# Kernel optimization log

Measured on AMD Instinct MI355X. Metric: run time of the kernel, lower is better.

## Reference

```python
import jax, jax.numpy as jnp
import numpy as np

E, H, V = 512, 1024, 32000
T_IN, T_DEC, B = 128, 128, 64
SOS = 1
WIPE_IDS = jnp.array([2, 3, 4])  # <EOS>, '\u56fe', '\u6298'


def gru_cell(x, h, Wih, Whh, bih, bhh):
    # torch nn.GRU cell math
    gi = x @ Wih.T + bih  # [B, 3H]
    gh = h @ Whh.T + bhh  # [B, 3H]
    i_r, i_z, i_n = jnp.split(gi, 3, axis=-1)
    h_r, h_z, h_n = jnp.split(gh, 3, axis=-1)
    r = jax.nn.sigmoid(i_r + h_r)
    z = jax.nn.sigmoid(i_z + h_z)
    n = jnp.tanh(i_n + r * h_n)
    return (1.0 - z) * n + z * h


def setup_inputs() -> dict:
    key = jax.random.key(0)
    ks = jax.random.split(key, 20)
    f = lambda k, shape: jax.random.normal(k, shape, jnp.float32) * 0.05
    inp = {
        'emb': f(ks[0], (V, E)),
        'enc_Wih': f(ks[1], (3 * H, E)), 'enc_Whh': f(ks[2], (3 * H, H)),
        'enc_bih': f(ks[3], (3 * H,)), 'enc_bhh': f(ks[4], (3 * H,)),
        'attn_W': f(ks[5], (T_IN, E + H)), 'attn_b': f(ks[6], (T_IN,)),
        'comb_W': f(ks[7], (H, E + H)), 'comb_b': f(ks[8], (H,)),
        'dec_Wih': f(ks[9], (3 * H, H)), 'dec_Whh': f(ks[10], (3 * H, H)),
        'dec_bih': f(ks[11], (3 * H,)), 'dec_bhh': f(ks[12], (3 * H,)),
        'out_W': f(ks[13], (V, H)), 'out_b': f(ks[14], (V,)),
        'src_tokens': jax.random.randint(ks[15], (B, T_IN), 0, V, jnp.int32),
        'tgt_tokens': jax.random.randint(ks[16], (B, T_DEC), 0, V, jnp.int32),
    }
    # pack_padded_sequence needs lengths sorted descending with max == T_IN
    sl = jax.random.randint(ks[17], (B,), 1, T_IN + 1, jnp.int32).at[0].set(T_IN)
    inp['src_lengths'] = jnp.sort(sl)[::-1]
    tl = jax.random.randint(ks[18], (B,), 1, T_DEC + 1, jnp.int32).at[0].set(T_DEC)
    inp['tgt_lengths'] = tl
    return inp


def reference(emb, enc_Wih, enc_Whh, enc_bih, enc_bhh, attn_W, attn_b,
              comb_W, comb_b, dec_Wih, dec_Whh, dec_bih, dec_bhh,
              out_W, out_b, src_tokens, src_lengths, tgt_tokens, tgt_lengths):
    # ---------------- Encoder (packed GRU semantics) ----------------
    x = emb[src_tokens]  # [B, T_IN, E]  (dropout is eval-mode identity)
    valid = jnp.arange(T_IN)[None, :] < src_lengths[:, None]  # [B, T_IN]

    def enc_step(h, inp):
        xt, vt = inp  # [B,E], [B]
        hn = gru_cell(xt, h, enc_Wih, enc_Whh, enc_bih, enc_bhh)
        h = jnp.where(vt[:, None], hn, h)          # freeze hidden past length
        out = jnp.where(vt[:, None], hn, 0.0)      # pad_packed zeros past length
        return h, out

    h0 = jnp.zeros((B, H), emb.dtype)
    enc_h, enc_out = jax.lax.scan(enc_step, h0, (x.transpose(1, 0, 2), valid.T))
    enc_out = enc_out.transpose(1, 0, 2)  # [B, T_IN, H]
    enc_out = jax.nn.log_softmax(enc_out, axis=1)  # LogSoftmax(dim=1) over time, as in source

    # ---------------- Attention decoder with teacher forcing ----------------
    sos = jnp.full((B,), SOS, src_tokens.dtype)

    def dec_step(carry, inp):
        h, prev = carry
        di, tgt_t = inp
        e = emb[prev]  # [B, E]
        union = jnp.concatenate([e, h], axis=-1)  # [B, E+H]
        aw = jax.nn.softmax(union @ attn_W.T + attn_b, axis=-1)  # [B, T_IN]
        info = jnp.einsum('bt,bth->bh', aw, enc_out)  # bmm
        comb = jax.nn.relu(jnp.concatenate([e, info], axis=-1) @ comb_W.T + comb_b)
        h = gru_cell(comb, h, dec_Wih, dec_Whh, dec_bih, dec_bhh)
        logits = h @ out_W.T + out_b  # [B, V]
        m = di < tgt_lengths  # [B] wipeEOS condition: now_len < length[i]
        wiped = jnp.where(m[:, None], 0.0, logits[:, WIPE_IDS])
        logits = logits.at[:, WIPE_IDS].set(wiped)
        pred_t = jnp.argmax(logits, axis=-1)
        ce = -jax.nn.log_softmax(logits, axis=-1)[jnp.arange(B), tgt_t]
        mf = m.astype(logits.dtype)
        step_loss = jnp.sum(ce * mf) / jnp.sum(mf)  # masked_select(...).mean()
        return (h, tgt_t), (pred_t, step_loss)

    (_, _), (preds, losses) = jax.lax.scan(
        dec_step, (enc_h, sos), (jnp.arange(T_DEC), tgt_tokens.T))
    return preds.T, jnp.sum(losses)
```

## Files before the change

kernel.cpp:

```cpp
#include <hip/hip_runtime.h>
#include <math.h>

typedef long long i64;

#define B_    64
#define TIN   128
#define TDEC  128
#define E_    512
#define H_    1024
#define V_    32000
#define H3    3072
#define EH    1536
#define NROWS 8192

__device__ inline unsigned int ordf(float v) {
  unsigned int u = __float_as_uint(v);
  return (u & 0x80000000u) ? ~u : (u | 0x80000000u);
}

__global__ void diag_fill(float* __restrict__ out, int n, float val) {
  int i = blockIdx.x * blockDim.x + threadIdx.x;
  if (i < n) out[i] = val;
}

__global__ void init_ws(float* __restrict__ hbuf, unsigned long long* __restrict__ amaxkey,
                        float* __restrict__ sumexp) {
  int i = blockIdx.x * blockDim.x + threadIdx.x;
  if (i < 2 * B_ * H_) hbuf[i] = 0.f;
  if (i < NROWS) { amaxkey[i] = 0ull; sumexp[i] = 0.f; }
}

__global__ void prep_tokens(const int* __restrict__ src, const int* __restrict__ tgt,
                            int* __restrict__ tok_src, int* __restrict__ tok_prev) {
  int r = blockIdx.x * blockDim.x + threadIdx.x;
  if (r >= NROWS) return;
  int t = r >> 6, b = r & 63;
  tok_src[r]  = src[b * TIN + t];
  tok_prev[r] = (t == 0) ? 1 : tgt[b * TDEC + (t - 1)];
}

__global__ __launch_bounds__(256)
void gemm_gather(const float* __restrict__ emb, const int* __restrict__ tok,
                 const float* __restrict__ W, int wstride,
                 const float* __restrict__ bias,
                 float* __restrict__ C, int ldc) {
  __shared__ float As[32][132];
  __shared__ float Bs[32][136];
  __shared__ int toks[128];
  const int tid = threadIdx.x;
  const int tx = tid & 15, ty = tid >> 4;
// ... 15 lines not shown
      As[k4 + 0][m] = v.x; As[k4 + 1][m] = v.y; As[k4 + 2][m] = v.z; As[k4 + 3][m] = v.w;
      float4 u = *reinterpret_cast<const float4*>(&W[(i64)(n0 + m) * wstride + k0 + k4]);
      Bs[k4 + 0][m] = u.x; Bs[k4 + 1][m] = u.y; Bs[k4 + 2][m] = u.z; Bs[k4 + 3][m] = u.w;
    }
    __syncthreads();
#pragma unroll
    for (int k = 0; k < 32; ++k) {
      float a[8], b[8];
      *(float4*)&a[0] = *(float4*)&As[k][ty * 4];
      *(float4*)&a[4] = *(float4*)&As[k][64 + ty * 4];
      *(float4*)&b[0] = *(float4*)&Bs[k][tx * 4];
      *(float4*)&b[4] = *(float4*)&Bs[k][64 + tx * 4];
#pragma unroll
      for (int i = 0; i < 8; ++i)
#pragma unroll
        for (int j = 0; j < 8; ++j)
          acc[i][j] = fmaf(a[i], b[j], acc[i][j]);
    }
    __syncthreads();
  }
#pragma unroll
  for (int i = 0; i < 8; ++i) {
    int rl = (i < 4) ? (ty * 4 + i) : (64 + ty * 4 + i - 4);
    int r = r0 + rl;
#pragma unroll
    for (int j = 0; j < 8; ++j) {
      int cl = (j < 4) ? (tx * 4 + j) : (64 + tx * 4 + j - 4);
      int c = n0 + cl;
      C[(i64)r * ldc + c] = acc[i][j] + bias[c];
    }
  }
}

template<int MODE>
__global__ __launch_bounds__(256)
void enc_step(const float* __restrict__ h_prev, float* __restrict__ h_next,
              const float* __restrict__ XGi,
              const float* __restrict__ emb, const int* __restrict__ src_tok,
              const float* __restrict__ Wih, const float* __restrict__ Whh,
              const float* __restrict__ bih, const float* __restrict__ bhh,
              const int* __restrict__ src_len,
              float* __restrict__ EncRaw, int t) {
  __shared__ float hs[64][66];
  __shared__ float Ws[3][8][66];
  __shared__ int toks[64];
  const int tid = threadIdx.x;
  const int n = tid & 7, q = tid >> 3;
  const int b0 = q * 2;
  const int n0 = blockIdx.x * 8;
  float gr0 = 0, gr1 = 0, gz0 = 0, gz1 = 0, gn0 = 0, gn1 = 0;
  float ir0 = 0, ir1 = 0, iz0 = 0, iz1 = 0, in0 = 0, in1 = 0;

  if (MODE == 1) {
    if (tid < 64) toks[tid] = src_tok[tid * TIN + t];
    __syncthreads();
    for (int k0 = 0; k0 < E_; k0 += 64) {
#pragma unroll
      for (int j = 0; j < 4; ++j) {
        int s = tid + 256 * j;
        int b = s >> 4, k4 = (s & 15) << 2;
        float4 v = *reinterpret_cast<const float4*>(&emb[(i64)toks[b] * E_ + k0 + k4]);
        hs[k4 + 0][b] = v.x; hs[k4 + 1][b] = v.y; hs[k4 + 2][b] = v.z; hs[k4 + 3][b] = v.w;
      }
#pragma unroll
      for (int j = 0; j < 2; ++j) {
        int s = tid + 256 * j;
        if (s < 384) {
          int g = s >> 7, s2 = s & 127;
          int nn = s2 >> 4, k4 = (s2 & 15) << 2;
          float4 v = *reinterpret_cast<const float4*>(&Wih[(i64)(g * H_ + n0 + nn) * E_ + k0 + k4]);
          Ws[g][nn][k4 + 0] = v.x; Ws[g][nn][k4 + 1] = v.y; Ws[g][nn][k4 + 2] = v.z; Ws[g][nn][k4 + 3] = v.w;
        }
      }
      __syncthreads();
#pragma unroll 16
      for (int k = 0; k < 64; ++k) {
        float2 xv = *reinterpret_cast<const float2*>(&hs[k][b0]);
        float w0 = Ws[0][n][k], w1 = Ws[1][n][k], w2 = Ws[2][n][k];
        ir0 = fmaf(xv.x, w0, ir0); ir1 = fmaf(xv.y, w0, ir1);
        iz0 = fmaf(xv.x, w1, iz0); iz1 = fmaf(xv.y, w1, iz1);
        in0 = fmaf(xv.x, w2, in0); in1 = fmaf(xv.y, w2, in1);
      }
      __syncthreads();
    }
  }

  for (int k0 = 0; k0 < H_; k0 += 64) {
#pragma unroll
    for (int j = 0; j < 4; ++j) {
      int s = tid + 256 * j;
      int b = s >> 4, k4 = (s & 15) << 2;
      float4 v = *reinterpret_cast<const float4*>(&h_prev[(i64)b * H_ + k0 + k4]);
      hs[k4 + 0][b] = v.x; hs[k4 + 1][b] = v.y; hs[k4 + 2][b] = v.z; hs[k4 + 3][b] = v.w;
    }
#pragma unroll
    for (int j = 0; j < 2; ++j) {
      int s = tid + 256 * j;
      if (s < 384) {
        int g = s >> 7, s2 = s & 127;
        int nn = s2 >> 4, k4 = (s2 & 15) << 2;
        float4 v = *reinterpret_cast<const float4*>(&Whh[(i64)(g * H_ + n0 + nn) * H_ + k0 + k4]);
        Ws[g][nn][k4 + 0] = v.x; Ws[g][nn][k4 + 1] = v.y; Ws[g][nn][k4 + 2] = v.z; Ws[g][nn][k4 + 3] = v.w;
      }
    }
    __syncthreads();
#pragma unroll 16
    for (int k = 0; k < 64; ++k) {
      float2 hv = *reinterpret_cast<const float2*>(&hs[k][b0]);
      float w0 = Ws[0][n][k], w1 = Ws[1][n][k], w2 = Ws[2][n][k];
      gr0 = fmaf(hv.x, w0, gr0); gr1 = fmaf(hv.y, w0, gr1);
      gz0 = fmaf(hv.x, w1, gz0); gz1 = fmaf(hv.y, w1, gz1);
      gn0 = fmaf(hv.x, w2, gn0); gn1 = fmaf(hv.y, w2, gn1);
    }
    __syncthreads();
  }

  const int col = n0 + n;
#pragma unroll
  for (int u = 0; u < 2; ++u) {
    int b = b0 + u;
    float gir, giz, gin;
    if (MODE == 0) {
      const float* g = &XGi[((i64)t * B_ + b) * H3];
      gir = g[col]; giz = g[H_ + col]; gin = g[2 * H_ + col];
    } else {
      gir = (u ? ir1 : ir0) + bih[col];
      giz = (u ? iz1 : iz0) + bih[H_ + col];
      gin = (u ? in1 : in0) + bih[2 * H_ + col];
    }
    float ghr = (u ? gr1 : gr0) + bhh[col];
    float ghz = (u ? gz1 : gz0) + bhh[H_ + col];
    float ghn = (u ? gn1 : gn0) + bhh[2 * H_ + col];
    float r = 1.f / (1.f + expf(-(gir + ghr)));
    float z = 1.f / (1.f + expf(-(giz + ghz)));
    float nn2 = tanhf(gin + r * ghn);
    float hp = h_prev[(i64)b * H_ + col];
    float hnew = (1.f - z) * nn2 + z * hp;
    bool valid = t < src_len[b];
    h_next[(i64)b * H_ + col] = valid ? hnew : hp;
    EncRaw[((i64)b * TIN + t) * H_ + col] = valid ? hnew : 0.f;
  }
}

__global__ void ls_time(float* __restrict__ Enc) {
  int idx = blockIdx.x * blockDim.x + threadIdx.x;
  int b = idx >> 10, c = idx & 1023;
  const i64 base = (i64)b * TIN * H_ + c;
  float M = -INFINITY;
  for (int t = 0; t < TIN; ++t) M = fmaxf(M, Enc[base + (i64)t * H_]);
  float S = 0.f;
  for (int t = 0; t < TIN; ++t) S += expf(Enc[base + (i64)t * H_] - M);
  float lg = M + logf(S);
  for (int t = 0; t < TIN; ++t) Enc[base + (i64)t * H_] -= lg;
}

__global__ __launch_bounds__(256)
void attn_info(const float* __restrict__ h_prev, const float* __restrict__ Ae,
               const float* __restrict__ attn_W, const float* __restrict__ EncLS,
               float* __restrict__ info, int t) {
  __shared__ float hl[H_];
  __shared__ float sc[TIN];
  const int b = blockIdx.x;
  const int tid = threadIdx.x;
  {
    float4 v = *reinterpret_cast<const float4*>(&h_prev[(i64)b * H_ + tid * 4]);
    *reinterpret_cast<float4*>(&hl[tid * 4]) = v;
  }
  __syncthreads();
  const int w = tid >> 6, lane = tid & 63;
  for (int si = 0; si < 32; ++si) {
    int s = w * 32 + si;
    float p = 0.f;
#pragma unroll
    for (int jj = 0; jj < 16; ++jj) {
      int j = jj * 64 + lane;
      p = fmaf(hl[j], attn_W[(i64)s * EH + E_ + j], p);
    }
#pragma unroll
    for (int off = 32; off > 0; off >>= 1) p += __shfl_down(p, off);
    if (lane == 0) sc[s] = p + Ae[((i64)t * B_ + b) * TIN + s];
  }
  __syncthreads();
  if (tid < 64) {
    float v0 = sc[tid], v1 = sc[tid + 64];
    float mx = fmaxf(v0, v1);
#pragma unroll
    for (int off = 32; off > 0; off >>= 1) mx = fmaxf(mx, __shfl_xor(mx, off));
    float e0 = expf(v0 - mx), e1 = expf(v1 - mx);
    float ss = e0 + e1;
#pragma unroll
    for (int off = 32; off > 0; off >>= 1) ss += __shfl_xor(ss, off);
    sc[tid] = e0 / ss; sc[tid + 64] = e1 / ss;
  }
  __syncthreads();
#pragma unroll
  for (int cc = 0; cc < 4; ++cc) {
    int c = tid + cc * 256;
    float acc = 0.f;
    for (int t2 = 0; t2 < TIN; ++t2)
      acc = fmaf(sc[t2], EncLS[((i64)b * TIN + t2) * H_ + c], acc);
    info[(i64)b * H_ + c] = acc;
  }
}

template<int MODE>
__global__ __launch_bounds__(256)
void comb_kernel(const float* __restrict__ info, const float* __restrict__ comb_W,
                 const float* __restrict__ Ce, const float* __restrict__ comb_b,
                 const float* __restrict__ emb, const int* __restrict__ tokP,
                 float* __restrict__ comb, int t) {
  __shared__ float is[64][68];
  __shared__ float Ws[16][66];
  __shared__ int toks[64];
  const int tid = threadIdx.x;
  const int n = tid & 15, q = tid >> 4;
  const int b0 = q * 4;
  const int n0 = blockIdx.x * 16;
  float a0 = 0, a1 = 0, a2 = 0, a3 = 0;

  if (MODE == 1) {
    if (tid < 64) toks[tid] = tokP[t * B_ + tid];
    __syncthreads();
    for (int k0 = 0; k0 < E_; k0 += 64) {
#pragma unroll
      for (int j = 0; j < 4; ++j) {
        int s = tid + 256 * j;
        int b = s >> 4, k4 = (s & 15) << 2;
        float4 v = *reinterpret_cast<const float4*>(&emb[(i64)toks[b] * E_ + k0 + k4]);
        is[k4 + 0][b] = v.x; is[k4 + 1][b] = v.y; is[k4 + 2][b] = v.z; is[k4 + 3][b] = v.w;
      }
      {
        int nn = tid >> 4, k4 = (tid & 15) << 2;
        float4 v = *reinterpret_cast<const float4*>(&comb_W[(i64)(n0 + nn) * EH + k0 + k4]);
        Ws[nn][k4 + 0] = v.x; Ws[nn][k4 + 1] = v.y; Ws[nn][k4 + 2] = v.z; Ws[nn][k4 + 3] = v.w;
      }
      __syncthreads();
#pragma unroll 16
      for (int k = 0; k < 64; ++k) {
        float4 iv = *reinterpret_cast<const float4*>(&is[k][b0]);
        float wv = Ws[n][k];
        a0 = fmaf(iv.x, wv, a0); a1 = fmaf(iv.y, wv, a1);
        a2 = fmaf(iv.z, wv, a2); a3 = fmaf(iv.w, wv, a3);
      }
      __syncthreads();
    }
  }

  for (int k0 = 0; k0 < H_; k0 += 64) {
#pragma unroll
    for (int j = 0; j < 4; ++j) {
      int s = tid + 256 * j;
      int b = s >> 4, k4 = (s & 15) << 2;
      float4 v = *reinterpret_cast<const float4*>(&info[(i64)b * H_ + k0 + k4]);
      is[k4 + 0][b] = v.x; is[k4 + 1][b] = v.y; is[k4 + 2][b] = v.z; is[k4 + 3][b] = v.w;
    }
    {
      int nn = tid >> 4, k4 = (tid & 15) << 2;
      float4 v = *reinterpret_cast<const float4*>(&comb_W[(i64)(n0 + nn) * EH + E_ + k0 + k4]);
      Ws[nn][k4 + 0] = v.x; Ws[nn][k4 + 1] = v.y; Ws[nn][k4 + 2] = v.z; Ws[nn][k4 + 3] = v.w;
    }
    __syncthreads();
#pragma unroll 16
    for (int k = 0; k < 64; ++k) {
      float4 iv = *reinterpret_cast<const float4*>(&is[k][b0]);
      float wv = Ws[n][k];
      a0 = fmaf(iv.x, wv, a0); a1 = fmaf(iv.y, wv, a1);
      a2 = fmaf(iv.z, wv, a2); a3 = fmaf(iv.w, wv, a3);
    }
    __syncthreads();
  }
  const int col = n0 + n;
#pragma unroll
  for (int u = 0; u < 4; ++u) {
    int b = b0 + u;
    float acc = (u == 0 ? a0 : u == 1 ? a1 : u == 2 ? a2 : a3);
    float base = (MODE == 0) ? Ce[((i64)t * B_ + b) * H_ + col] : comb_b[col];
    float v = base + acc;
    comb[(i64)b * H_ + col] = fmaxf(v, 0.f);
  }
}

__global__ __launch_bounds__(256)
void dec_gru(const float* __restrict__ h_prev, const float* __restrict__ comb,
             const float* __restrict__ Wih, const float* __restrict__ Whh,
             const float* __restrict__ bih, const float* __restrict__ bhh,
             float* __restrict__ h_out) {
  __shared__ float hs[64][66];
  __shared__ float cs[64][66];
  __shared__ float Wh[3][8][66];
  __shared__ float Wi[3][8][66];
  const int tid = threadIdx.x;
  const int n = tid & 7, q = tid >> 3;
  const int b0 = q * 2;
  const int n0 = blockIdx.x * 8;
  float sr0 = 0, sr1 = 0, sz0 = 0, sz1 = 0, gin0 = 0, gin1 = 0, ghn0 = 0, ghn1 = 0;
  for (int k0 = 0; k0 < H_; k0 += 64) {
#pragma unroll
    for (int j = 0; j < 4; ++j) {
      int s = tid + 256 * j;
      int b = s >> 4, k4 = (s & 15) << 2;
      float4 v = *reinterpret_cast<const float4*>(&h_prev[(i64)b * H_ + k0 + k4]);
      hs[k4 + 0][b] = v.x; hs[k4 + 1][b] = v.y; hs[k4 + 2][b] = v.z; hs[k4 + 3][b] = v.w;
      float4 u = *reinterpret_cast<const float4*>(&comb[(i64)b * H_ + k0 + k4]);
      cs[k4 + 0][b] = u.x; cs[k4 + 1][b] = u.y; cs[k4 + 2][b] = u.z; cs[k4 + 3][b] = u.w;
    }
#pragma unroll
    for (int j = 0; j < 2; ++j) {
      int s = tid + 256 * j;
      if (s < 384) {
        int g = s >> 7, s2 = s & 127;
        int nn = s2 >> 4, k4 = (s2 & 15) << 2;
        float4 v = *reinterpret_cast<const float4*>(&Whh[(i64)(g * H_ + n0 + nn) * H_ + k0 + k4]);
        Wh[g][nn][k4 + 0] = v.x; Wh[g][nn][k4 + 1] = v.y; Wh[g][nn][k4 + 2] = v.z; Wh[g][nn][k4 + 3] = v.w;
        float4 u = *reinterpret_cast<const float4*>(&Wih[(i64)(g * H_ + n0 + nn) * H_ + k0 + k4]);
        Wi[g][nn][k4 + 0] = u.x; Wi[g][nn][k4 + 1] = u.y; Wi[g][nn][k4 + 2] = u.z; Wi[g][nn][k4 + 3] = u.w;
      }
    }
    __syncthreads();
#pragma unroll 8
    for (int k = 0; k < 64; ++k) {
      float2 hv = *reinterpret_cast<const float2*>(&hs[k][b0]);
      float2 cv = *reinterpret_cast<const float2*>(&cs[k][b0]);
      float whr = Wh[0][n][k], whz = Wh[1][n][k], whn = Wh[2][n][k];
      float wir = Wi[0][n][k], wiz = Wi[1][n][k], win = Wi[2][n][k];
      sr0 = fmaf(hv.x, whr, sr0); sr0 = fmaf(cv.x, wir, sr0);
      sr1 = fmaf(hv.y, whr, sr1); sr1 = fmaf(cv.y, wir, sr1);
      sz0 = fmaf(hv.x, whz, sz0); sz0 = fmaf(cv.x, wiz, sz0);
      sz1 = fmaf(hv.y, whz, sz1); sz1 = fmaf(cv.y, wiz, sz1);
      gin0 = fmaf(cv.x, win, gin0); gin1 = fmaf(cv.y, win, gin1);
      ghn0 = fmaf(hv.x, whn, ghn0); ghn1 = fmaf(hv.y, whn, ghn1);
    }
    __syncthreads();
  }
  const int col = n0 + n;
#pragma unroll
  for (int u = 0; u < 2; ++u) {
    int b = b0 + u;
    float r = 1.f / (1.f + expf(-((u ? sr1 : sr0) + bih[col] + bhh[col])));
    float z = 1.f / (1.f + expf(-((u ? sz1 : sz0) + bih[H_ + col] + bhh[H_ + col])));
    float nn2 = tanhf((u ? gin1 : gin0) + bih[2 * H_ + col] + r * ((u ? ghn1 : ghn0) + bhh[2 * H_ + col]));
    float hp = h_prev[(i64)b * H_ + col];
    h_out[(i64)b * H_ + col] = (1.f - z) * nn2 + z * hp;
  }
}

__global__ __launch_bounds__(256)
void logits_fused(const float* __restrict__ A, const float* __restrict__ Wout,
                  const float* __restrict__ outb, const int* __restrict__ tlen,
                  unsigned long long* __restrict__ amaxkey, float* __restrict__ sumexp) {
  __shared__ float As[32][132];
  __shared__ float Bs[32][136];
  __shared__ float redm[128][17];
  __shared__ int   redi[128][17];
  __shared__ float reds[128][17];
  const int tid = threadIdx.x;
  const int tx = tid & 15, ty = tid >> 4;
  const int r0 = blockIdx.y * 128, n0 = blockIdx.x * 128;
  float acc[8][8];
#pragma unroll
  for (int i = 0; i < 8; ++i)
#pragma unroll
    for (int j = 0; j < 8; ++j) acc[i][j] = 0.f;

  for (int k0 = 0; k0 < H_; k0 += 32) {
#pragma unroll
    for (int j = 0; j < 4; ++j) {
      int s = tid + 256 * j;
      int m = s >> 3, k4 = (s & 7) << 2;
      float4 v = *reinterpret_cast<const float4*>(&A[(i64)(r0 + m) * H_ + k0 + k4]);
      As[k4 + 0][m] = v.x; As[k4 + 1][m] = v.y; As[k4 + 2][m] = v.z; As[k4 + 3][m] = v.w;
      float4 u = *reinterpret_cast<const float4*>(&Wout[(i64)(n0 + m) * H_ + k0 + k4]);
      Bs[k4 + 0][m] = u.x; Bs[k4 + 1][m] = u.y; Bs[k4 + 2][m] = u.z; Bs[k4 + 3][m] = u.w;
    }
    __syncthreads();
#pragma unroll
    for (int k = 0; k < 32; ++k) {
      float a[8], b[8];
      *(float4*)&a[0] = *(float4*)&As[k][ty * 4];
      *(float4*)&a[4] = *(float4*)&As[k][64 + ty * 4];
      *(float4*)&b[0] = *(float4*)&Bs[k][tx * 4];
      *(float4*)&b[4] = *(float4*)&Bs[k][64 + tx * 4];
#pragma unroll
      for (int i = 0; i < 8; ++i)
#pragma unroll
        for (int j = 0; j < 8; ++j)
          acc[i][j] = fmaf(a[i], b[j], acc[i][j]);
    }
    __syncthreads();
  }

  int cols[8], rloc[8];
#pragma unroll
  for (int j = 0; j < 8; ++j) cols[j] = n0 + ((j < 4) ? (tx * 4 + j) : (64 + tx * 4 + j - 4));
#pragma unroll
  for (int i = 0; i < 8; ++i) rloc[i] = (i < 4) ? (ty * 4 + i) : (64 + ty * 4 + i - 4);

#pragma unroll
  for (int i = 0; i < 8; ++i) {
    int r = r0 + rloc[i];
    int t = r >> 6, b = r & 63;
    bool m = t < tlen[b];
    float lm = -INFINITY; int li = 0x7fffffff; float ls = 0.f;
#pragma unroll
    for (int j = 0; j < 8; ++j) {
      float v = acc[i][j] + outb[cols[j]];
      if (m && cols[j] >= 2 && cols[j] <= 4) v = 0.f;
      ls += expf(v);
      if (v > lm || (v == lm && cols[j] < li)) { lm = v; li = cols[j]; }
    }
    redm[rloc[i]][tx] = lm; redi[rloc[i]][tx] = li; reds[rloc[i]][tx] = ls;
  }
  __syncthreads();
  if (tid < 128) {
    float M = -INFINITY; int I = 0x7fffffff; float S = 0.f;
#pragma unroll
    for (int x = 0; x < 16; ++x) {
      float v = redm[tid][x]; int id = redi[tid][x];
      if (v > M || (v == M && id < I)) { M = v; I = id; }
      S += reds[tid][x];
    }
    unsigned long long key = ((unsigned long long)ordf(M) << 32) | (0xFFFFFFFFu - (unsigned)I);
    atomicMax(&amaxkey[r0 + tid], key);
    atomicAdd(&sumexp[r0 + tid], S);
  }
}

__global__ void tlogit_kernel(const float* __restrict__ Hd, const float* __restrict__ Wout,
                              const float* __restrict__ outb, const int* __restrict__ tgt,
                              const int* __restrict__ tlen, float* __restrict__ tlog) {
  const int tid = threadIdx.x;
  const int w = tid >> 6, lane = tid & 63;
  const int r = blockIdx.x * 4 + w;
  const int t = r >> 6, b = r & 63;
  const int tg = tgt[b * TDEC + t];
  float p = 0.f;
#pragma unroll
  for (int jj = 0; jj < 16; ++jj) {
    int j = jj * 64 + lane;
    p = fmaf(Hd[(i64)r * H_ + j], Wout[(i64)tg * H_ + j], p);
  }
#pragma unroll
  for (int off = 32; off > 0; off >>= 1) p += __shfl_down(p, off);
  if (lane == 0) {
    float v = p + outb[tg];
    if ((t < tlen[b]) && tg >= 2 && tg <= 4) v = 0.f;
    tlog[r] = v;
  }
}

__global__ void merge_kernel(const unsigned long long* __restrict__ amaxkey,
                             const float* __restrict__ sumexp,
                             const float* __restrict__ tlog,
// ... 52 lines not shown
  const int* tgt_len;
  if (in_sizes[16] == B_ * TDEC) {
    tgt_tok = (const int*)d_in[16];
    src_len = (const int*)d_in[17];
    tgt_len = (const int*)d_in[18];
  } else {
    src_len = (const int*)d_in[16];
    tgt_len = (const int*)d_in[17];
    tgt_tok = (const int*)d_in[18];
  }
  float* out = (float*)d_out;
  char* wsb = (char*)d_ws;
  size_t off = 0;
  auto alloc = [&](size_t bytes) { void* p = wsb + off; off += (bytes + 255) & ~(size_t)255; return p; };

  float* EncLS = (float*)alloc((size_t)NROWS * H_ * 4);
  float* hbuf  = (float*)alloc(2ull * B_ * H_ * 4);
  float* Ae    = (float*)alloc((size_t)NROWS * TIN * 4);
  float* Hdec  = (float*)alloc((size_t)NROWS * H_ * 4);
  float* info  = (float*)alloc((size_t)B_ * H_ * 4);
  float* comb  = (float*)alloc((size_t)B_ * H_ * 4);
  unsigned long long* amaxkey = (unsigned long long*)alloc((size_t)NROWS * 8);
  float* sumexp = (float*)alloc((size_t)NROWS * 4);
  float* tlog  = (float*)alloc((size_t)NROWS * 4);
  float* lossT = (float*)alloc(TDEC * 4);
  int* tokS    = (int*)alloc(NROWS * 4);
  int* tokP    = (int*)alloc(NROWS * 4);

  if (off > ws_size) {
    diag_fill<<<(out_size + 255) / 256, 256, 0, stream>>>(out, out_size, (float)ws_size);
    return;
  }

  const size_t CeB  = (size_t)NROWS * H_ * 4;
  const size_t XGiB = (size_t)NROWS * H3 * 4;
  float* Ce  = nullptr;
  float* XGi = nullptr;
  if (ws_size >= off + CeB + 256)  Ce  = (float*)alloc(CeB);
  if (ws_size >= off + XGiB + 256) XGi = (float*)alloc(XGiB);

  init_ws<<<512, 256, 0, stream>>>(hbuf, amaxkey, sumexp);
  prep_tokens<<<32, 256, 0, stream>>>(src_tok, tgt_tok, tokS, tokP);
  if (XGi)
    gemm_gather<<<dim3(24, 64), 256, 0, stream>>>(emb, tokS, enc_Wih, E_, enc_bih, XGi, H3);
  gemm_gather<<<dim3(1, 64), 256, 0, stream>>>(emb, tokP, attn_W, EH, attn_b, Ae, TIN);
  if (Ce)
    gemm_gather<<<dim3(8, 64), 256, 0, stream>>>(emb, tokP, comb_W, EH, comb_b, Ce, H_);

  for (int t = 0; t < TIN; ++t) {
    const float* hp = hbuf + (size_t)(t & 1) * (B_ * H_);
    float* hn = hbuf + (size_t)((t + 1) & 1) * (B_ * H_);
    if (XGi)
      enc_step<0><<<128, 256, 0, stream>>>(hp, hn, XGi, emb, src_tok, enc_Wih, enc_Whh,
                                           enc_bih, enc_bhh, src_len, EncLS, t);
    else
      enc_step<1><<<128, 256, 0, stream>>>(hp, hn, nullptr, emb, src_tok, enc_Wih, enc_Whh,
                                           enc_bih, enc_bhh, src_len, EncLS, t);
  }
  ls_time<<<256, 256, 0, stream>>>(EncLS);

  for (int t = 0; t < TDEC; ++t) {
    const float* hp = (t == 0) ? hbuf : (Hdec + (i64)(t - 1) * B_ * H_);
    attn_info<<<64, 256, 0, stream>>>(hp, Ae, attn_W, EncLS, info, t);
    if (Ce)
      comb_kernel<0><<<64, 256, 0, stream>>>(info, comb_W, Ce, comb_b, emb, tokP, comb, t);
    else
      comb_kernel<1><<<64, 256, 0, stream>>>(info, comb_W, nullptr, comb_b, emb, tokP, comb, t);
    dec_gru<<<128, 256, 0, stream>>>(hp, comb, dec_Wih, dec_Whh, dec_bih, dec_bhh,
                                     Hdec + (i64)t * B_ * H_);
  }

  logits_fused<<<dim3(250, 64), 256, 0, stream>>>(Hdec, out_W, out_b, tgt_len, amaxkey, sumexp);
  tlogit_kernel<<<2048, 256, 0, stream>>>(Hdec, out_W, out_b, tgt_tok, tgt_len, tlog);
  merge_kernel<<<128, 64, 0, stream>>>(amaxkey, sumexp, tlog, tgt_len, out, lossT);
  loss_sum<<<1, 128, 0, stream>>>(lossT, out);
}
```

Measured before the change: 34.72 ms.

## Re-split recurrent encoder/decoder step kernels across more blocks with split-K reduction

```diff
diff --git a/kernel.cpp b/kernel.cpp
--- a/kernel.cpp
+++ b/kernel.cpp
@@ -12,10 +12,22 @@
 #define H3    3072
 #define EH    1536
 #define NROWS 8192
+#define BH    (B_ * H_)
 
 __device__ inline unsigned int ordf(float v) {
   unsigned int u = __float_as_uint(v);
   return (u & 0x80000000u) ? ~u : (u | 0x80000000u);
+}
+
+__device__ __forceinline__ void fma16(float acc[4][4], float4 s, float4 w) {
+  acc[0][0] = fmaf(s.x, w.x, acc[0][0]); acc[0][1] = fmaf(s.x, w.y, acc[0][1]);
+  acc[0][2] = fmaf(s.x, w.z, acc[0][2]); acc[0][3] = fmaf(s.x, w.w, acc[0][3]);
+  acc[1][0] = fmaf(s.y, w.x, acc[1][0]); acc[1][1] = fmaf(s.y, w.y, acc[1][1]);
+  acc[1][2] = fmaf(s.y, w.z, acc[1][2]); acc[1][3] = fmaf(s.y, w.w, acc[1][3]);
+  acc[2][0] = fmaf(s.z, w.x, acc[2][0]); acc[2][1] = fmaf(s.z, w.y, acc[2][1]);
+  acc[2][2] = fmaf(s.z, w.z, acc[2][2]); acc[2][3] = fmaf(s.z, w.w, acc[2][3]);
+  acc[3][0] = fmaf(s.w, w.x, acc[3][0]); acc[3][1] = fmaf(s.w, w.y, acc[3][1]);
+  acc[3][2] = fmaf(s.w, w.z, acc[3][2]); acc[3][3] = fmaf(s.w, w.w, acc[3][3]);
 }
 
 __global__ void diag_fill(float* __restrict__ out, int n, float val) {
@@ -97,112 +109,84 @@
   }
 }
 
-template<int MODE>
-__global__ __launch_bounds__(256)
-void enc_step(const float* __restrict__ h_prev, float* __restrict__ h_next,
-              const float* __restrict__ XGi,
-              const float* __restrict__ emb, const int* __restrict__ src_tok,
-              const float* __restrict__ Wih, const float* __restrict__ Whh,
-              const float* __restrict__ bih, const float* __restrict__ bhh,
-              const int* __restrict__ src_len,
-              float* __restrict__ EncRaw, int t) {
-  __shared__ float hs[64][66];
-  __shared__ float Ws[3][8][66];
+__global__ __launch_bounds__(512)
+void enc_step2(const float* __restrict__ h_prev, float* __restrict__ h_next,
+               const float* __restrict__ emb, const int* __restrict__ tokS,
+               const float* __restrict__ Wih, const float* __restrict__ Whh,
+               const float* __restrict__ bih, const float* __restrict__ bhh,
+               const int* __restrict__ src_len, float* __restrict__ EncRaw, int t) {
+  __shared__ float S[64][68];
+  __shared__ float WL[64 * 32];
+  __shared__ float red[8 * 1024];
   __shared__ int toks[64];
   const int tid = threadIdx.x;
-  const int n = tid & 7, q = tid >> 3;
-  const int b0 = q * 2;
-  const int n0 = blockIdx.x * 8;
-  float gr0 = 0, gr1 = 0, gz0 = 0, gz1 = 0, gn0 = 0, gn1 = 0;
-  float ir0 = 0, ir1 = 0, iz0 = 0, iz1 = 0, in0 = 0, in1 = 0;
-
-  if (MODE == 1) {
-    if (tid < 64) toks[tid] = src_tok[tid * TIN + t];
-    __syncthreads();
-    for (int k0 = 0; k0 < E_; k0 += 64) {
-#pragma unroll
-      for (int j = 0; j < 4; ++j) {
-        int s = tid + 256 * j;
-        int b = s >> 4, k4 = (s & 15) << 2;
-        float4 v = *reinterpret_cast<const float4*>(&emb[(i64)toks[b] * E_ + k0 + k4]);
-        hs[k4 + 0][b] = v.x; hs[k4 + 1][b] = v.y; hs[k4 + 2][b] = v.z; hs[k4 + 3][b] = v.w;
+  const int n0 = blockIdx.x * 4;
+  const int bg = tid & 15, ac = (tid >> 4) & 3, ks = tid >> 6;
+  const int b0 = bg * 4;
+  if (tid < 64) toks[tid] = tokS[t * B_ + tid];
+  float acc[4][4] = {{0}};
+  for (int ch = 0; ch < 24; ++ch) {
+    const bool isE = ch < 8;
+    const int k0 = (isE ? ch : ch - 8) * 64;
+    __syncthreads();
+    {
+      int b = tid & 63, kb = (tid >> 6) * 8;
+      const float* src = isE ? &emb[(i64)toks[b] * E_ + k0 + kb]
+                             : &h_prev[(i64)b * H_ + k0 + kb];
+      float4 v0 = *(const float4*)src;
+      float4 v1 = *(const float4*)(src + 4);
+      S[kb + 0][b] = v0.x; S[kb + 1][b] = v0.y; S[kb + 2][b] = v0.z; S[kb + 3][b] = v0.w;
+      S[kb + 4][b] = v1.x; S[kb + 5][b] = v1.y; S[kb + 6][b] = v1.z; S[kb + 7][b] = v1.w;
+    }
+    if (tid < 192) {
+      int lin = tid * 4;
+      int row12 = lin >> 6, k4 = lin & 63;
+      int m = row12 >> 2, c = row12 & 3;
+      const float* W = isE ? Wih : Whh;
+      const int K = isE ? E_ : H_;
+      float4 w = *(const float4*)&W[(i64)(m * H_ + n0 + c) * K + k0 + k4];
+      int slot = ((m ^ ((k4 >> 2) & 7)) << 2) + c;
+      WL[(k4 + 0) * 32 + slot] = w.x;
+      WL[(k4 + 1) * 32 + slot] = w.y;
+      WL[(k4 + 2) * 32 + slot] = w.z;
+      WL[(k4 + 3) * 32 + slot] = w.w;
+    }
+    __syncthreads();
+    const bool active = (ac < 2) || (ac == 2 && isE) || (ac == 3 && !isE);
+    if (active) {
+      const int m = (ac < 2) ? ac : 2;
+#pragma unroll
+      for (int kk = ks * 8; kk < ks * 8 + 8; ++kk) {
+        float4 sv = *(float4*)&S[kk][b0];
+        float4 wv = *(float4*)&WL[kk * 32 + ((m ^ ((kk >> 2) & 7)) << 2)];
+        fma16(acc, sv, wv);
       }
-#pragma unroll
-      for (int j = 0; j < 2; ++j) {
-        int s = tid + 256 * j;
-        if (s < 384) {
-          int g = s >> 7, s2 = s & 127;
-          int nn = s2 >> 4, k4 = (s2 & 15) << 2;
-          float4 v = *reinterpret_cast<const float4*>(&Wih[(i64)(g * H_ + n0 + nn) * E_ + k0 + k4]);
-          Ws[g][nn][k4 + 0] = v.x; Ws[g][nn][k4 + 1] = v.y; Ws[g][nn][k4 + 2] = v.z; Ws[g][nn][k4 + 3] = v.w;
-        }
-      }
-      __syncthreads();
-#pragma unroll 16
-      for (int k = 0; k < 64; ++k) {
-        float2 xv = *reinterpret_cast<const float2*>(&hs[k][b0]);
-        float w0 = Ws[0][n][k], w1 = Ws[1][n][k], w2 = Ws[2][n][k];
-        ir0 = fmaf(xv.x, w0, ir0); ir1 = fmaf(xv.y, w0, ir1);
-        iz0 = fmaf(xv.x, w1, iz0); iz1 = fmaf(xv.y, w1, iz1);
-        in0 = fmaf(xv.x, w2, in0); in1 = fmaf(xv.y, w2, in1);
-      }
-      __syncthreads();
-    }
-  }
-
-  for (int k0 = 0; k0 < H_; k0 += 64) {
-#pragma unroll
-    for (int j = 0; j < 4; ++j) {
-      int s = tid + 256 * j;
-      int b = s >> 4, k4 = (s & 15) << 2;
-      float4 v = *reinterpret_cast<const float4*>(&h_prev[(i64)b * H_ + k0 + k4]);
-      hs[k4 + 0][b] = v.x; hs[k4 + 1][b] = v.y; hs[k4 + 2][b] = v.z; hs[k4 + 3][b] = v.w;
-    }
-#pragma unroll
-    for (int j = 0; j < 2; ++j) {
-      int s = tid + 256 * j;
-      if (s < 384) {
-        int g = s >> 7, s2 = s & 127;
-        int nn = s2 >> 4, k4 = (s2 & 15) << 2;
-        float4 v = *reinterpret_cast<const float4*>(&Whh[(i64)(g * H_ + n0 + nn) * H_ + k0 + k4]);
-        Ws[g][nn][k4 + 0] = v.x; Ws[g][nn][k4 + 1] = v.y; Ws[g][nn][k4 + 2] = v.z; Ws[g][nn][k4 + 3] = v.w;
-      }
-    }
-    __syncthreads();
-#pragma unroll 16
-    for (int k = 0; k < 64; ++k) {
-      float2 hv = *reinterpret_cast<const float2*>(&hs[k][b0]);
-      float w0 = Ws[0][n][k], w1 = Ws[1][n][k], w2 = Ws[2][n][k];
-      gr0 = fmaf(hv.x, w0, gr0); gr1 = fmaf(hv.y, w0, gr1);
-      gz0 = fmaf(hv.x, w1, gz0); gz1 = fmaf(hv.y, w1, gz1);
-      gn0 = fmaf(hv.x, w2, gn0); gn1 = fmaf(hv.y, w2, gn1);
-    }
-    __syncthreads();
-  }
-
-  const int col = n0 + n;
-#pragma unroll
-  for (int u = 0; u < 2; ++u) {
-    int b = b0 + u;
-    float gir, giz, gin;
-    if (MODE == 0) {
-      const float* g = &XGi[((i64)t * B_ + b) * H3];
-      gir = g[col]; giz = g[H_ + col]; gin = g[2 * H_ + col];
-    } else {
-      gir = (u ? ir1 : ir0) + bih[col];
-      giz = (u ? iz1 : iz0) + bih[H_ + col];
-      gin = (u ? in1 : in0) + bih[2 * H_ + col];
-    }
-    float ghr = (u ? gr1 : gr0) + bhh[col];
-    float ghz = (u ? gz1 : gz0) + bhh[H_ + col];
-    float ghn = (u ? gn1 : gn0) + bhh[2 * H_ + col];
-    float r = 1.f / (1.f + expf(-(gir + ghr)));
-    float z = 1.f / (1.f + expf(-(giz + ghz)));
-    float nn2 = tanhf(gin + r * ghn);
-    float hp = h_prev[(i64)b * H_ + col];
-    float hnew = (1.f - z) * nn2 + z * hp;
+    }
+  }
+  __syncthreads();
+#pragma unroll
+  for (int bi = 0; bi < 4; ++bi)
+#pragma unroll
+    for (int c = 0; c < 4; ++c)
+      red[ks * 1024 + ac * 256 + c * 64 + b0 + bi] = acc[bi][c];
+  __syncthreads();
+  if (tid < 256) {
+    int b = tid & 63, c = tid >> 6, col = n0 + c;
+    float sr = 0, sz = 0, gin = 0, ghn = 0;
+#pragma unroll
+    for (int k2 = 0; k2 < 8; ++k2) {
+      sr  += red[k2 * 1024 +   0 + c * 64 + b];
+      sz  += red[k2 * 1024 + 256 + c * 64 + b];
+      gin += red[k2 * 1024 + 512 + c * 64 + b];
+      ghn += red[k2 * 1024 + 768 + c * 64 + b];
+    }
+    float r = 1.f / (1.f + expf(-(sr + bih[col] + bhh[col])));
+    float z = 1.f / (1.f + expf(-(sz + bih[H_ + col] + bhh[H_ + col])));
+    float nn = tanhf(gin + bih[2 * H_ + col] + r * (ghn + bhh[2 * H_ + col]));
+    float hpv = h_prev[(i64)b * H_ + col];
+    float hnew = (1.f - z) * nn + z * hpv;
     bool valid = t < src_len[b];
-    h_next[(i64)b * H_ + col] = valid ? hnew : hp;
+    h_next[(i64)b * H_ + col] = valid ? hnew : hpv;
     EncRaw[((i64)b * TIN + t) * H_ + col] = valid ? hnew : 0.f;
   }
 }
@@ -219,22 +203,24 @@
   for (int t = 0; t < TIN; ++t) Enc[base + (i64)t * H_] -= lg;
 }
 
-__global__ __launch_bounds__(256)
-void attn_info(const float* __restrict__ h_prev, const float* __restrict__ Ae,
-               const float* __restrict__ attn_W, const float* __restrict__ EncLS,
-               float* __restrict__ info, int t) {
+__global__ __launch_bounds__(512)
+void attn_info2(const float* __restrict__ h_prev, const float* __restrict__ Ae,
+                const float* __restrict__ attn_W, const float* __restrict__ EncLS,
+                float* __restrict__ info, int t) {
   __shared__ float hl[H_];
   __shared__ float sc[TIN];
-  const int b = blockIdx.x;
-  const int tid = threadIdx.x;
-  {
-    float4 v = *reinterpret_cast<const float4*>(&h_prev[(i64)b * H_ + tid * 4]);
-    *reinterpret_cast<float4*>(&hl[tid * 4]) = v;
+  __shared__ float inf2[512];
+  const int b = blockIdx.x & 63, quarter = blockIdx.x >> 6;
+  const int tid = threadIdx.x;
+  if (tid < 256) {
+    float4 v = *(const float4*)&h_prev[(i64)b * H_ + tid * 4];
+    *(float4*)&hl[tid * 4] = v;
   }
   __syncthreads();
   const int w = tid >> 6, lane = tid & 63;
-  for (int si = 0; si < 32; ++si) {
-    int s = w * 32 + si;
+#pragma unroll
+  for (int si = 0; si < 16; ++si) {
+    int s = w * 16 + si;
     float p = 0.f;
 #pragma unroll
     for (int jj = 0; jj < 16; ++jj) {
@@ -258,154 +244,173 @@
     sc[tid] = e0 / ss; sc[tid + 64] = e1 / ss;
   }
   __syncthreads();
-#pragma unroll
-  for (int cc = 0; cc < 4; ++cc) {
-    int c = tid + cc * 256;
+  {
+    int c = quarter * 256 + (tid & 255);
+    int th = tid >> 8;
     float acc = 0.f;
-    for (int t2 = 0; t2 < TIN; ++t2)
+    for (int t2 = th * 64; t2 < th * 64 + 64; ++t2)
       acc = fmaf(sc[t2], EncLS[((i64)b * TIN + t2) * H_ + c], acc);
-    info[(i64)b * H_ + c] = acc;
-  }
-}
-
-template<int MODE>
-__global__ __launch_bounds__(256)
-void comb_kernel(const float* __restrict__ info, const float* __restrict__ comb_W,
-                 const float* __restrict__ Ce, const float* __restrict__ comb_b,
-                 const float* __restrict__ emb, const int* __restrict__ tokP,
-                 float* __restrict__ comb, int t) {
-  __shared__ float is[64][68];
-  __shared__ float Ws[16][66];
+    inf2[tid] = acc;
+    __syncthreads();
+    if (th == 0) info[(i64)b * H_ + c] = acc + inf2[tid + 256];
+  }
+}
+
+__global__ __launch_bounds__(512)
+void comb2(const float* __restrict__ info, const float* __restrict__ emb,
+           const int* __restrict__ tokP, const float* __restrict__ comb_W,
+           const float* __restrict__ comb_b, float* __restrict__ comb, int t) {
+  __shared__ float S[64][68];
+  __shared__ float WB[64 * 20];
+  __shared__ float red[8 * 256];
   __shared__ int toks[64];
   const int tid = threadIdx.x;
-  const int n = tid & 15, q = tid >> 4;
-  const int b0 = q * 4;
-  const int n0 = blockIdx.x * 16;
-  float a0 = 0, a1 = 0, a2 = 0, a3 = 0;
-
-  if (MODE == 1) {
-    if (tid < 64) toks[tid] = tokP[t * B_ + tid];
-    __syncthreads();
-    for (int k0 = 0; k0 < E_; k0 += 64) {
-#pragma unroll
-      for (int j = 0; j < 4; ++j) {
-        int s = tid + 256 * j;
-        int b = s >> 4, k4 = (s & 15) << 2;
-        float4 v = *reinterpret_cast<const float4*>(&emb[(i64)toks[b] * E_ + k0 + k4]);
-        is[k4 + 0][b] = v.x; is[k4 + 1][b] = v.y; is[k4 + 2][b] = v.z; is[k4 + 3][b] = v.w;
+  const int n0 = blockIdx.x * 4;
+  const int bg = tid & 15, cs = (tid >> 4) & 3, ks = tid >> 6;
+  const int b0 = bg * 4;
+  if (tid < 64) toks[tid] = tokP[t * B_ + tid];
+  float acc[4] = {0, 0, 0, 0};
+  for (int ch = 0; ch < 24; ++ch) {
+    const bool isE = ch < 8;
+    const int k0 = (isE ? ch : ch - 8) * 64;
+    __syncthreads();
+    {
+      int b = tid & 63, kb = (tid >> 6) * 8;
+      const float* src = isE ? &emb[(i64)toks[b] * E_ + k0 + kb]
+                             : &info[(i64)b * H_ + k0 + kb];
+      float4 v0 = *(const float4*)src;
+      float4 v1 = *(const float4*)(src + 4);
+      S[kb + 0][b] = v0.x; S[kb + 1][b] = v0.y; S[kb + 2][b] = v0.z; S[kb + 3][b] = v0.w;
+      S[kb + 4][b] = v1.x; S[kb + 5][b] = v1.y; S[kb + 6][b] = v1.z; S[kb + 7][b] = v1.w;
+    }
+    if (tid < 64) {
+      int k = tid;
+      i64 koff = (i64)(isE ? 0 : E_) + k0 + k;
+      float4 w;
+      w.x = comb_W[(i64)(n0 + 0) * EH + koff];
+      w.y = comb_W[(i64)(n0 + 1) * EH + koff];
+      w.z = comb_W[(i64)(n0 + 2) * EH + koff];
+      w.w = comb_W[(i64)(n0 + 3) * EH + koff];
+      *(float4*)&WB[k * 20] = w;
+    }
+    __syncthreads();
+#pragma unroll
+    for (int kk = ks * 8; kk < ks * 8 + 8; ++kk) {
+      float4 sv = *(float4*)&S[kk][b0];
+      float wv = WB[kk * 20 + cs];
+      acc[0] = fmaf(sv.x, wv, acc[0]);
+      acc[1] = fmaf(sv.y, wv, acc[1]);
+      acc[2] = fmaf(sv.z, wv, acc[2]);
+      acc[3] = fmaf(sv.w, wv, acc[3]);
+    }
+  }
+  __syncthreads();
+#pragma unroll
+  for (int bi = 0; bi < 4; ++bi)
+    red[ks * 256 + cs * 64 + b0 + bi] = acc[bi];
+  __syncthreads();
+  if (tid < 256) {
+    int b = tid & 63, c = tid >> 6;
+    float s = comb_b[n0 + c];
+#pragma unroll
+    for (int k2 = 0; k2 < 8; ++k2) s += red[k2 * 256 + c * 64 + b];
+    comb[(i64)b * H_ + n0 + c] = fmaxf(s, 0.f);
+  }
+}
+
+__global__ __launch_bounds__(512)
+void dec_gru2(const float* __restrict__ h_prev, const float* __restrict__ comb,
+              const float* __restrict__ Wih, const float* __restrict__ Whh,
+              const float* __restrict__ bih, const float* __restrict__ bhh,
+              float* __restrict__ h_out) {
+  __shared__ float S1[64][68];
+  __shared__ float S2[64][68];
+  __shared__ float WL[64 * 32];
+  __shared__ float red[8 * 1024];
+  const int tid = threadIdx.x;
+  const int n0 = blockIdx.x * 4;
+  const int bg = tid & 15, ac = (tid >> 4) & 3, ks = tid >> 6;
+  const int b0 = bg * 4;
+  float acc[4][4] = {{0}};
+  for (int ch = 0; ch < 16; ++ch) {
+    const int k0 = ch * 64;
+    __syncthreads();
+    {
+      int b = tid & 63, kb = (tid >> 6) * 8;
+      const float* s1 = &h_prev[(i64)b * H_ + k0 + kb];
+      const float* s2 = &comb[(i64)b * H_ + k0 + kb];
+      float4 v0 = *(const float4*)s1, v1 = *(const float4*)(s1 + 4);
+      S1[kb + 0][b] = v0.x; S1[kb + 1][b] = v0.y; S1[kb + 2][b] = v0.z; S1[kb + 3][b] = v0.w;
+      S1[kb + 4][b] = v1.x; S1[kb + 5][b] = v1.y; S1[kb + 6][b] = v1.z; S1[kb + 7][b] = v1.w;
+      float4 u0 = *(const float4*)s2, u1 = *(const float4*)(s2 + 4);
+      S2[kb + 0][b] = u0.x; S2[kb + 1][b] = u0.y; S2[kb + 2][b] = u0.z; S2[kb + 3][b] = u0.w;
+      S2[kb + 4][b] = u1.x; S2[kb + 5][b] = u1.y; S2[kb + 6][b] = u1.z; S2[kb + 7][b] = u1.w;
+    }
+    if (tid < 384) {
+      int lin = tid * 4;
+      int row24 = lin >> 6, k4 = lin & 63;
+      int m = row24 >> 2, c = row24 & 3;
+      int g = m >> 1;
+      const float* W = (m & 1) ? Wih : Whh;
+      float4 w = *(const float4*)&W[(i64)(g * H_ + n0 + c) * H_ + k0 + k4];
+      int slot = ((m ^ ((k4 >> 2) & 7)) << 2) + c;
+      WL[(k4 + 0) * 32 + slot] = w.x;
+      WL[(k4 + 1) * 32 + slot] = w.y;
+      WL[(k4 + 2) * 32 + slot] = w.z;
+      WL[(k4 + 3) * 32 + slot] = w.w;
+    }
+    __syncthreads();
+    if (ac < 2) {
+#pragma unroll
+      for (int kk = ks * 8; kk < ks * 8 + 8; ++kk) {
+        int key = (kk >> 2) & 7;
+        float4 h4 = *(float4*)&S1[kk][b0];
+        float4 c4 = *(float4*)&S2[kk][b0];
+        float4 wh = *(float4*)&WL[kk * 32 + (((2 * ac) ^ key) << 2)];
+        float4 wi = *(float4*)&WL[kk * 32 + (((2 * ac + 1) ^ key) << 2)];
+        fma16(acc, h4, wh);
+        fma16(acc, c4, wi);
       }
-      {
-        int nn = tid >> 4, k4 = (tid & 15) << 2;
-        float4 v = *reinterpret_cast<const float4*>(&comb_W[(i64)(n0 + nn) * EH + k0 + k4]);
-        Ws[nn][k4 + 0] = v.x; Ws[nn][k4 + 1] = v.y; Ws[nn][k4 + 2] = v.z; Ws[nn][k4 + 3] = v.w;
+    } else if (ac == 2) {
+#pragma unroll
+      for (int kk = ks * 8; kk < ks * 8 + 8; ++kk) {
+        int key = (kk >> 2) & 7;
+        float4 c4 = *(float4*)&S2[kk][b0];
+        float4 wi = *(float4*)&WL[kk * 32 + ((5 ^ key) << 2)];
+        fma16(acc, c4, wi);
       }
-      __syncthreads();
-#pragma unroll 16
-      for (int k = 0; k < 64; ++k) {
-        float4 iv = *reinterpret_cast<const float4*>(&is[k][b0]);
-        float wv = Ws[n][k];
-        a0 = fmaf(iv.x, wv, a0); a1 = fmaf(iv.y, wv, a1);
-        a2 = fmaf(iv.z, wv, a2); a3 = fmaf(iv.w, wv, a3);
+    } else {
+#pragma unroll
+      for (int kk = ks * 8; kk < ks * 8 + 8; ++kk) {
+        int key = (kk >> 2) & 7;
+        float4 h4 = *(float4*)&S1[kk][b0];
+        float4 wh = *(float4*)&WL[kk * 32 + ((4 ^ key) << 2)];
+        fma16(acc, h4, wh);
       }
-      __syncthreads();
-    }
-  }
-
-  for (int k0 = 0; k0 < H_; k0 += 64) {
-#pragma unroll
-    for (int j = 0; j < 4; ++j) {
-      int s = tid + 256 * j;
-      int b = s >> 4, k4 = (s & 15) << 2;
-      float4 v = *reinterpret_cast<const float4*>(&info[(i64)b * H_ + k0 + k4]);
-      is[k4 + 0][b] = v.x; is[k4 + 1][b] = v.y; is[k4 + 2][b] = v.z; is[k4 + 3][b] = v.w;
-    }
-    {
-      int nn = tid >> 4, k4 = (tid & 15) << 2;
-      float4 v = *reinterpret_cast<const float4*>(&comb_W[(i64)(n0 + nn) * EH + E_ + k0 + k4]);
-      Ws[nn][k4 + 0] = v.x; Ws[nn][k4 + 1] = v.y; Ws[nn][k4 + 2] = v.z; Ws[nn][k4 + 3] = v.w;
-    }
-    __syncthreads();
-#pragma unroll 16
-    for (int k = 0; k < 64; ++k) {
-      float4 iv = *reinterpret_cast<const float4*>(&is[k][b0]);
-      float wv = Ws[n][k];
-      a0 = fmaf(iv.x, wv, a0); a1 = fmaf(iv.y, wv, a1);
-      a2 = fmaf(iv.z, wv, a2); a3 = fmaf(iv.w, wv, a3);
-    }
-    __syncthreads();
-  }
-  const int col = n0 + n;
-#pragma unroll
-  for (int u = 0; u < 4; ++u) {
-    int b = b0 + u;
-    float acc = (u == 0 ? a0 : u == 1 ? a1 : u == 2 ? a2 : a3);
-    float base = (MODE == 0) ? Ce[((i64)t * B_ + b) * H_ + col] : comb_b[col];
-    float v = base + acc;
-    comb[(i64)b * H_ + col] = fmaxf(v, 0.f);
-  }
-}
-
-__global__ __launch_bounds__(256)
-void dec_gru(const float* __restrict__ h_prev, const float* __restrict__ comb,
-             const float* __restrict__ Wih, const float* __restrict__ Whh,
-             const float* __restrict__ bih, const float* __restrict__ bhh,
-             float* __restrict__ h_out) {
-  __shared__ float hs[64][66];
-  __shared__ float cs[64][66];
-  __shared__ float Wh[3][8][66];
-  __shared__ float Wi[3][8][66];
-  const int tid = threadIdx.x;
-  const int n = tid & 7, q = tid >> 3;
-  const int b0 = q * 2;
-  const int n0 = blockIdx.x * 8;
-  float sr0 = 0, sr1 = 0, sz0 = 0, sz1 = 0, gin0 = 0, gin1 = 0, ghn0 = 0, ghn1 = 0;
-  for (int k0 = 0; k0 < H_; k0 += 64) {
-#pragma unroll
-    for (int j = 0; j < 4; ++j) {
-      int s = tid + 256 * j;
-      int b = s >> 4, k4 = (s & 15) << 2;
-      float4 v = *reinterpret_cast<const float4*>(&h_prev[(i64)b * H_ + k0 + k4]);
-      hs[k4 + 0][b] = v.x; hs[k4 + 1][b] = v.y; hs[k4 + 2][b] = v.z; hs[k4 + 3][b] = v.w;
-      float4 u = *reinterpret_cast<const float4*>(&comb[(i64)b * H_ + k0 + k4]);
-      cs[k4 + 0][b] = u.x; cs[k4 + 1][b] = u.y; cs[k4 + 2][b] = u.z; cs[k4 + 3][b] = u.w;
-    }
-#pragma unroll
-    for (int j = 0; j < 2; ++j) {
-      int s = tid + 256 * j;
-      if (s < 384) {
-        int g = s >> 7, s2 = s & 127;
-        int nn = s2 >> 4, k4 = (s2 & 15) << 2;
-        float4 v = *reinterpret_cast<const float4*>(&Whh[(i64)(g * H_ + n0 + nn) * H_ + k0 + k4]);
-        Wh[g][nn][k4 + 0] = v.x; Wh[g][nn][k4 + 1] = v.y; Wh[g][nn][k4 + 2] = v.z; Wh[g][nn][k4 + 3] = v.w;
-        float4 u = *reinterpret_cast<const float4*>(&Wih[(i64)(g * H_ + n0 + nn) * H_ + k0 + k4]);
-        Wi[g][nn][k4 + 0] = u.x; Wi[g][nn][k4 + 1] = u.y; Wi[g][nn][k4 + 2] = u.z; Wi[g][nn][k4 + 3] = u.w;
-      }
-    }
-    __syncthreads();
-#pragma unroll 8
-    for (int k = 0; k < 64; ++k) {
-      float2 hv = *reinterpret_cast<const float2*>(&hs[k][b0]);
-      float2 cv = *reinterpret_cast<const float2*>(&cs[k][b0]);
-      float whr = Wh[0][n][k], whz = Wh[1][n][k], whn = Wh[2][n][k];
-      float wir = Wi[0][n][k], wiz = Wi[1][n][k], win = Wi[2][n][k];
-      sr0 = fmaf(hv.x, whr, sr0); sr0 = fmaf(cv.x, wir, sr0);
-      sr1 = fmaf(hv.y, whr, sr1); sr1 = fmaf(cv.y, wir, sr1);
-      sz0 = fmaf(hv.x, whz, sz0); sz0 = fmaf(cv.x, wiz, sz0);
-      sz1 = fmaf(hv.y, whz, sz1); sz1 = fmaf(cv.y, wiz, sz1);
-      gin0 = fmaf(cv.x, win, gin0); gin1 = fmaf(cv.y, win, gin1);
-      ghn0 = fmaf(hv.x, whn, ghn0); ghn1 = fmaf(hv.y, whn, ghn1);
-    }
-    __syncthreads();
-  }
-  const int col = n0 + n;
-#pragma unroll
-  for (int u = 0; u < 2; ++u) {
-    int b = b0 + u;
-    float r = 1.f / (1.f + expf(-((u ? sr1 : sr0) + bih[col] + bhh[col])));
-    float z = 1.f / (1.f + expf(-((u ? sz1 : sz0) + bih[H_ + col] + bhh[H_ + col])));
-    float nn2 = tanhf((u ? gin1 : gin0) + bih[2 * H_ + col] + r * ((u ? ghn1 : ghn0) + bhh[2 * H_ + col]));
-    float hp = h_prev[(i64)b * H_ + col];
-    h_out[(i64)b * H_ + col] = (1.f - z) * nn2 + z * hp;
+    }
+  }
+  __syncthreads();
+#pragma unroll
+  for (int bi = 0; bi < 4; ++bi)
+#pragma unroll
+    for (int c = 0; c < 4; ++c)
+      red[ks * 1024 + ac * 256 + c * 64 + b0 + bi] = acc[bi][c];
+  __syncthreads();
+  if (tid < 256) {
+    int b = tid & 63, c = tid >> 6, col = n0 + c;
+    float sr = 0, sz = 0, gin = 0, ghn = 0;
+#pragma unroll
+    for (int k2 = 0; k2 < 8; ++k2) {
+      sr  += red[k2 * 1024 +   0 + c * 64 + b];
+      sz  += red[k2 * 1024 + 256 + c * 64 + b];
+      gin += red[k2 * 1024 + 512 + c * 64 + b];
+      ghn += red[k2 * 1024 + 768 + c * 64 + b];
+    }
+    float r = 1.f / (1.f + expf(-(sr + bih[col] + bhh[col])));
+    float z = 1.f / (1.f + expf(-(sz + bih[H_ + col] + bhh[H_ + col])));
+    float nn = tanhf(gin + bih[2 * H_ + col] + r * (ghn + bhh[2 * H_ + col]));
+    float hpv = h_prev[(i64)b * H_ + col];
+    h_out[(i64)b * H_ + col] = (1.f - z) * nn + z * hpv;
   }
 }
 
@@ -413,11 +418,10 @@
 void logits_fused(const float* __restrict__ A, const float* __restrict__ Wout,
                   const float* __restrict__ outb, const int* __restrict__ tlen,
                   unsigned long long* __restrict__ amaxkey, float* __restrict__ sumexp) {
-  __shared__ float As[32][132];
-  __shared__ float Bs[32][136];
-  __shared__ float redm[128][17];
-  __shared__ int   redi[128][17];
-  __shared__ float reds[128][17];
+  __shared__ union {
+    struct { float As[32][132]; float Bs[32][136]; } g;
+    struct { float redm[128][17]; int redi[128][17]; float reds[128][17]; } r;
+  } sh;
   const int tid = threadIdx.x;
   const int tx = tid & 15, ty = tid >> 4;
   const int r0 = blockIdx.y * 128, n0 = blockIdx.x * 128;
@@ -433,18 +437,20 @@
       int s = tid + 256 * j;
       int m = s >> 3, k4 = (s & 7) << 2;
       float4 v = *reinterpret_cast<const float4*>(&A[(i64)(r0 + m) * H_ + k0 + k4]);
-      As[k4 + 0][m] = v.x; As[k4 + 1][m] = v.y; As[k4 + 2][m] = v.z; As[k4 + 3][m] = v.w;
+      sh.g.As[k4 + 0][m] = v.x; sh.g.As[k4 + 1][m] = v.y;
+      sh.g.As[k4 + 2][m] = v.z; sh.g.As[k4 + 3][m] = v.w;
       float4 u = *reinterpret_cast<const float4*>(&Wout[(i64)(n0 + m) * H_ + k0 + k4]);
-      Bs[k4 + 0][m] = u.x; Bs[k4 + 1][m] = u.y; Bs[k4 + 2][m] = u.z; Bs[k4 + 3][m] = u.w;
+      sh.g.Bs[k4 + 0][m] = u.x; sh.g.Bs[k4 + 1][m] = u.y;
+      sh.g.Bs[k4 + 2][m] = u.z; sh.g.Bs[k4 + 3][m] = u.w;
     }
     __syncthreads();
 #pragma unroll
     for (int k = 0; k < 32; ++k) {
       float a[8], b[8];
-      *(float4*)&a[0] = *(float4*)&As[k][ty * 4];
-      *(float4*)&a[4] = *(float4*)&As[k][64 + ty * 4];
-      *(float4*)&b[0] = *(float4*)&Bs[k][tx * 4];
-      *(float4*)&b[4] = *(float4*)&Bs[k][64 + tx * 4];
+      *(float4*)&a[0] = *(float4*)&sh.g.As[k][ty * 4];
+      *(float4*)&a[4] = *(float4*)&sh.g.As[k][64 + ty * 4];
+      *(float4*)&b[0] = *(float4*)&sh.g.Bs[k][tx * 4];
+      *(float4*)&b[4] = *(float4*)&sh.g.Bs[k][64 + tx * 4];
 #pragma unroll
       for (int i = 0; i < 8; ++i)
 #pragma unroll
@@ -473,16 +479,16 @@
       ls += expf(v);
       if (v > lm || (v == lm && cols[j] < li)) { lm = v; li = cols[j]; }
     }
-    redm[rloc[i]][tx] = lm; redi[rloc[i]][tx] = li; reds[rloc[i]][tx] = ls;
+    sh.r.redm[rloc[i]][tx] = lm; sh.r.redi[rloc[i]][tx] = li; sh.r.reds[rloc[i]][tx] = ls;
   }
   __syncthreads();
   if (tid < 128) {
     float M = -INFINITY; int I = 0x7fffffff; float S = 0.f;
 #pragma unroll
     for (int x = 0; x < 16; ++x) {
-      float v = redm[tid][x]; int id = redi[tid][x];
+      float v = sh.r.redm[tid][x]; int id = sh.r.redi[tid][x];
       if (v > M || (v == M && id < I)) { M = v; I = id; }
-      S += reds[tid][x];
+      S += sh.r.reds[tid][x];
     }
     unsigned long long key = ((unsigned long long)ordf(M) << 32) | (0xFFFFFFFFu - (unsigned)I);
     atomicMax(&amaxkey[r0 + tid], key);
@@ -601,42 +607,24 @@
     return;
   }
 
-  const size_t CeB  = (size_t)NROWS * H_ * 4;
-  const size_t XGiB = (size_t)NROWS * H3 * 4;
-  float* Ce  = nullptr;
-  float* XGi = nullptr;
-  if (ws_size >= off + CeB + 256)  Ce  = (float*)alloc(CeB);
-  if (ws_size >= off + XGiB + 256) XGi = (float*)alloc(XGiB);
-
   init_ws<<<512, 256, 0, stream>>>(hbuf, amaxkey, sumexp);
   prep_tokens<<<32, 256, 0, stream>>>(src_tok, tgt_tok, tokS, tokP);
-  if (XGi)
-    gemm_gather<<<dim3(24, 64), 256, 0, stream>>>(emb, tokS, enc_Wih, E_, enc_bih, XGi, H3);
   gemm_gather<<<dim3(1, 64), 256, 0, stream>>>(emb, tokP, attn_W, EH, attn_b, Ae, TIN);
-  if (Ce)
-    gemm_gather<<<dim3(8, 64), 256, 0, stream>>>(emb, tokP, comb_W, EH, comb_b, Ce, H_);
 
   for (int t = 0; t < TIN; ++t) {
-    const float* hp = hbuf + (size_t)(t & 1) * (B_ * H_);
-    float* hn = hbuf + (size_t)((t + 1) & 1) * (B_ * H_);
-    if (XGi)
-      enc_step<0><<<128, 256, 0, stream>>>(hp, hn, XGi, emb, src_tok, enc_Wih, enc_Whh,
-                                           enc_bih, enc_bhh, src_len, EncLS, t);
-    else
-      enc_step<1><<<128, 256, 0, stream>>>(hp, hn, nullptr, emb, src_tok, enc_Wih, enc_Whh,
-                                           enc_bih, enc_bhh, src_len, EncLS, t);
+    const float* hp = hbuf + (size_t)(t & 1) * BH;
+    float* hn = hbuf + (size_t)((t + 1) & 1) * BH;
+    enc_step2<<<256, 512, 0, stream>>>(hp, hn, emb, tokS, enc_Wih, enc_Whh,
+                                       enc_bih, enc_bhh, src_len, EncLS, t);
   }
   ls_time<<<256, 256, 0, stream>>>(EncLS);
 
   for (int t = 0; t < TDEC; ++t) {
-    const float* hp = (t == 0) ? hbuf : (Hdec + (i64)(t - 1) * B_ * H_);
-    attn_info<<<64, 256, 0, stream>>>(hp, Ae, attn_W, EncLS, info, t);
-    if (Ce)
-      comb_kernel<0><<<64, 256, 0, stream>>>(info, comb_W, Ce, comb_b, emb, tokP, comb, t);
-    else
-      comb_kernel<1><<<64, 256, 0, stream>>>(info, comb_W, nullptr, comb_b, emb, tokP, comb, t);
-    dec_gru<<<128, 256, 0, stream>>>(hp, comb, dec_Wih, dec_Whh, dec_bih, dec_bhh,
-                                     Hdec + (i64)t * B_ * H_);
+    const float* hp = (t == 0) ? hbuf : (Hdec + (i64)(t - 1) * BH);
+    attn_info2<<<256, 512, 0, stream>>>(hp, Ae, attn_W, EncLS, info, t);
+    comb2<<<256, 512, 0, stream>>>(info, emb, tokP, comb_W, comb_b, comb, t);
+    dec_gru2<<<256, 512, 0, stream>>>(hp, comb, dec_Wih, dec_Whh, dec_bih, dec_bhh,
+                                      Hdec + (i64)t * BH);
   }
 
   logits_fused<<<dim3(250, 64), 256, 0, stream>>>(Hdec, out_W, out_b, tgt_len, amaxkey, sumexp);
```

Result: slower. 36.11 ms (+4.0%).
